# Performance work log

Hardware: AMD Instinct MI355X
Metric: run time of the kernel (lower is better)

The kernel has to match this reference:

```python
import jax, jax.numpy as jnp
import numpy as np

N = 20000      # nodes
E = 320000     # edges (avg degree 16)
S = 2          # extra feature axis (mean-pooled before fc)
IN = 128       # in_feats
H = 246        # n_hidden (must be 246 to match fc = Linear(246, 1))


def setup_inputs() -> dict:
    key = jax.random.key(0)
    ks = jax.random.split(key, 8)
    feat = jax.random.normal(ks[0], (N, S, IN), jnp.float32)
    src = jax.random.randint(ks[1], (E,), 0, N, jnp.int32)
    dst = jax.random.randint(ks[2], (E,), 0, N, jnp.int32)
    glorot = lambda k, shp, fan: jax.random.normal(k, shp, jnp.float32) / np.sqrt(fan).astype(np.float32)
    return {
        "features": feat,
        "src": src,
        "dst": dst,
        "W0": glorot(ks[3], (IN, H), IN), "b0": jnp.zeros((H,), jnp.float32),
        "W1": glorot(ks[4], (H, H), H),   "b1": jnp.zeros((H,), jnp.float32),
        "W2": glorot(ks[5], (H, H), H),   "b2": jnp.zeros((H,), jnp.float32),
        "fc_w": glorot(ks[6], (H, 1), H), "fc_b": jnp.zeros((1,), jnp.float32),
    }


def reference(features, src, dst, W0, b0, W1, b1, W2, b2, fc_w, fc_b):
    # DGL GraphConv, norm='both': h' = act( D_in^{-1/2} A D_out^{-1/2} h W + b )
    ones = jnp.ones((src.shape[0],), jnp.float32)
    out_deg = jax.ops.segment_sum(ones, src, num_segments=N)
    in_deg = jax.ops.segment_sum(ones, dst, num_segments=N)
    norm_out = jax.lax.rsqrt(jnp.maximum(out_deg, 1.0))[:, None, None]  # [N,1,1]
    norm_in = jax.lax.rsqrt(jnp.maximum(in_deg, 1.0))[:, None, None]

    def graph_conv(h, W, b):
        h = h * norm_out                                      # [N,S,F] scale by src-side norm
        agg = jax.ops.segment_sum(h[src], dst, num_segments=N)  # gather->scatter-add over edges
        agg = agg * norm_in
        return jax.nn.relu(agg @ W + b)

    h = graph_conv(features.astype(jnp.float32), W0, b0)
    # dropout between layers is identity in eval mode
    h = graph_conv(h, W1, b1)
    h = graph_conv(h, W2, b2)
    return h.mean(axis=1) @ fc_w + fc_b  # [N,1]
```

## Files before the change

kernel.cpp:

```cpp
#include <hip/hip_runtime.h>
#include <hip/hip_fp16.h>

#define NN 20000
#define NE 320000
#define SS 2
#define FIN 128
#define FH 246

typedef _Float16 f16x8 __attribute__((ext_vector_type(8)));
typedef float f32x4 __attribute__((ext_vector_type(4)));

__global__ void degree_kernel(const int* __restrict__ src, const int* __restrict__ dst,
                              int* __restrict__ deg_out, int* __restrict__ deg_in) {
    int e = blockIdx.x * blockDim.x + threadIdx.x;
    if (e < NE) {
        atomicAdd(&deg_out[src[e]], 1);
        atomicAdd(&deg_in[dst[e]], 1);
    }
}

__global__ void norm_kernel(const int* __restrict__ deg_out, const int* __restrict__ deg_in,
                            float* __restrict__ norm_out, float* __restrict__ norm_in) {
    int n = blockIdx.x * blockDim.x + threadIdx.x;
    if (n < NN) {
        norm_out[n] = rsqrtf(fmaxf((float)deg_out[n], 1.0f));
        norm_in[n]  = rsqrtf(fmaxf((float)deg_in[n], 1.0f));
    }
}

__global__ void alloc_kernel(const int* __restrict__ deg_in, int* __restrict__ row_start,
                             int* __restrict__ cursor, int* __restrict__ counter) {
    __shared__ int smem[256];
    __shared__ int base_s;
    int tid = threadIdx.x;
    int i = blockIdx.x * 256 + tid;
    int v = (i < NN) ? deg_in[i] : 0;
    smem[tid] = v;
    __syncthreads();
    for (int off = 1; off < 256; off <<= 1) {
        int t = (tid >= off) ? smem[tid - off] : 0;
        __syncthreads();
        smem[tid] += t;
        __syncthreads();
    }
    int incl = smem[tid];
    if (tid == 0) base_s = atomicAdd(counter, smem[255]);
    __syncthreads();
    if (i < NN) {
        int excl = base_s + incl - v;
        row_start[i] = excl;
        cursor[i]    = excl;
    }
}

__global__ void scatter_kernel(const int* __restrict__ src, const int* __restrict__ dst,
                               int* __restrict__ cursor, int* __restrict__ sorted_src) {
    int e = blockIdx.x * blockDim.x + threadIdx.x;
    if (e < NE) {
        int d = dst[e];
        int pos = atomicAdd(&cursor[d], 1);
        sorted_src[pos] = src[e];
    }
}

__global__ void convert_w_split(const float* __restrict__ W,
                                ushort* __restrict__ Wh, ushort* __restrict__ Wl, int K) {
    int n = blockIdx.x, k = threadIdx.x;
    float v = (k < K && n < 246) ? W[k * 246 + n] : 0.f;
    _Float16 h = (_Float16)v;
    _Float16 l = (_Float16)(v - (float)h);
    Wh[n * 256 + k] = *(ushort*)&h;
    Wl[n * 256 + k] = *(ushort*)&l;
}

__global__ void init_out(float* __restrict__ out, const float* __restrict__ fcb) {
    int i = blockIdx.x * 256 + threadIdx.x;
    if (i < NN) out[i] = fcb[0];
}

template<int F4ROW>
__global__ void aggregate2(const float* __restrict__ h,
                           const int* __restrict__ row_start,
                           const int* __restrict__ deg_in,
                           const int* __restrict__ sorted_src,
                           const float* __restrict__ norm_out,
                           const float* __restrict__ norm_in,
                           ushort* __restrict__ Ah, ushort* __restrict__ Al) {
    int g  = threadIdx.x >> 5;
    int l  = threadIdx.x & 31;
    int n  = blockIdx.x * 4 + g;
    if (n >= NN) return;
    int idx = blockIdx.y * 32 + l;
    const float4* hv = (const float4*)h;
    int beg = row_start[n];
    int end = beg + deg_in[n];
    float4 acc = {0.f, 0.f, 0.f, 0.f};
    int i = beg;
    for (; i + 4 <= end; i += 4) {
        int s0 = sorted_src[i + 0];
        int s1 = sorted_src[i + 1];
        int s2 = sorted_src[i + 2];
        int s3 = sorted_src[i + 3];
        float n0 = norm_out[s0], n1 = norm_out[s1];
        float n2 = norm_out[s2], n3 = norm_out[s3];
        float4 v0 = hv[(size_t)s0 * F4ROW + idx];
        float4 v1 = hv[(size_t)s1 * F4ROW + idx];
        float4 v2 = hv[(size_t)s2 * F4ROW + idx];
        float4 v3 = hv[(size_t)s3 * F4ROW + idx];
        acc.x += v0.x * n0 + v1.x * n1 + v2.x * n2 + v3.x * n3;
        acc.y += v0.y * n0 + v1.y * n1 + v2.y * n2 + v3.y * n3;
        acc.z += v0.z * n0 + v1.z * n1 + v2.z * n2 + v3.z * n3;
        acc.w += v0.w * n0 + v1.w * n1 + v2.w * n2 + v3.w * n3;
    }
    for (; i < end; ++i) {
        int s = sorted_src[i];
        float nr = norm_out[s];
        float4 v = hv[(size_t)s * F4ROW + idx];
        acc.x += v.x * nr;
        acc.y += v.y * nr;
        acc.z += v.z * nr;
        acc.w += v.w * nr;
    }
    float ni = norm_in[n];
    float v[4] = {acc.x * ni, acc.y * ni, acc.z * ni, acc.w * ni};
    ushort hp[4], lp[4];
#pragma unroll
    for (int j = 0; j < 4; ++j) {
        _Float16 hh = (_Float16)v[j];
        _Float16 ll = (_Float16)(v[j] - (float)hh);
        hp[j] = *(ushort*)&hh;
        lp[j] = *(ushort*)&ll;
    }
    ((uint2*)Ah)[(size_t)n * F4ROW + idx] = *(uint2*)hp;
    ((uint2*)Al)[(size_t)n * F4ROW + idx] = *(uint2*)lp;
}

template<int KP, bool FUSE>
__global__ __launch_bounds__(256) void gemm_split(const ushort* __restrict__ Ah,
                                                  const ushort* __restrict__ Al,
                                                  const ushort* __restrict__ Wh,
                                                  const ushort* __restrict__ Wl,
                                                  const float* __restrict__ b,
                                                  void* __restrict__ outv,
                                                  const float* __restrict__ fcw) {
    constexpr int NT = KP / 32;
    constexpr int AS = KP / 8;
    __shared__ __align__(16) _Float16 Ah_s[64][40];
    __shared__ __align__(16) _Float16 Al_s[64][40];
    __shared__ __align__(16) _Float16 Bh_s[128][40];
    __shared__ __align__(16) _Float16 Bl_s[128][40];

    int tid  = threadIdx.x;
    int m0   = blockIdx.x * 64;
    int n0   = blockIdx.y * 128;
    int wave = tid >> 6, lane = tid & 63;
    int wm = wave >> 1, wn = wave & 1;
    int lr = lane & 15, quad = lane >> 4;

    f32x4 acc[2][4];
#pragma unroll
    for (int mi = 0; mi < 2; ++mi)
#pragma unroll
        for (int ni = 0; ni < 4; ++ni) acc[mi][ni] = {0.f, 0.f, 0.f, 0.f};

    int ar = tid >> 2;
    int aq = tid & 3;
    const uint4* Ahv = (const uint4*)Ah;
    const uint4* Alv = (const uint4*)Al;
    const uint4* Whv = (const uint4*)Wh;
    const uint4* Wlv = (const uint4*)Wl;

    for (int t0 = 0; t0 < NT; ++t0) {
        size_t abase = (size_t)(m0 + ar) * AS + t0 * 4 + aq;
        *(uint4*)&Ah_s[ar][aq * 8] = Ahv[abase];
        *(uint4*)&Al_s[ar][aq * 8] = Alv[abase];
#pragma unroll
        for (int it = 0; it < 2; ++it) {
            int f = it * 256 + tid;
            int rn = f >> 2, q = f & 3;
            size_t base = (size_t)(n0 + rn) * 32 + t0 * 4 + q;
            *(uint4*)&Bh_s[rn][q * 8] = Whv[base];
            *(uint4*)&Bl_s[rn][q * 8] = Wlv[base];
        }
        __syncthreads();

        f16x8 ah[2], al[2], bh[4], bl[4];
#pragma unroll
        for (int mi = 0; mi < 2; ++mi) {
            ah[mi] = *(const f16x8*)&Ah_s[wm * 32 + mi * 16 + lr][quad * 8];
            al[mi] = *(const f16x8*)&Al_s[wm * 32 + mi * 16 + lr][quad * 8];
        }
#pragma unroll
        for (int ni = 0; ni < 4; ++ni) {
            bh[ni] = *(const f16x8*)&Bh_s[wn * 64 + ni * 16 + lr][quad * 8];
            bl[ni] = *(const f16x8*)&Bl_s[wn * 64 + ni * 16 + lr][quad * 8];
        }
#pragma unroll
        for (int mi = 0; mi < 2; ++mi)
#pragma unroll
            for (int ni = 0; ni < 4; ++ni) {
                acc[mi][ni] = __builtin_amdgcn_mfma_f32_16x16x32_f16(ah[mi], bh[ni], acc[mi][ni], 0, 0, 0);
                acc[mi][ni] = __builtin_amdgcn_mfma_f32_16x16x32_f16(al[mi], bh[ni], acc[mi][ni], 0, 0, 0);
                acc[mi][ni] = __builtin_amdgcn_mfma_f32_16x16x32_f16(ah[mi], bl[ni], acc[mi][ni], 0, 0, 0);
            }
        __syncthreads();
    }

    if (FUSE) {
        float* out = (float*)outv;
#pragma unroll
        for (int mi = 0; mi < 2; ++mi) {
#pragma unroll
            for (int i = 0; i < 4; ++i) {
                float p = 0.f;
#pragma unroll
                for (int ni = 0; ni < 4; ++ni) {
                    int c = n0 + wn * 64 + ni * 16 + lr;
                    if (c < 246)
                        p += fmaxf(acc[mi][ni][i] + b[c], 0.f) * fcw[c];
                }
#pragma unroll
                for (int off = 8; off > 0; off >>= 1)
                    p += __shfl_down(p, off, 16);
                if (lr == 0) {
                    int m = m0 + wm * 32 + mi * 16 + quad * 4 + i;
                    atomicAdd(&out[m >> 1], 0.5f * p);
                }
            }
        }
    } else {
        float* outF = (float*)outv;
#pragma unroll
        for (int ni = 0; ni < 4; ++ni) {
            int c = n0 + wn * 64 + ni * 16 + lr;
            float bj = (c < 246) ? b[c] : 0.f;
#pragma unroll
            for (int mi = 0; mi < 2; ++mi)
#pragma unroll
                for (int i = 0; i < 4; ++i) {
                    int m = m0 + wm * 32 + mi * 16 + quad * 4 + i;
                    outF[(size_t)m * 256 + c] = fmaxf(acc[mi][ni][i] + bj, 0.f);
                }
        }
    }
}

extern "C" void kernel_launch(void* const* d_in, const int* in_sizes, int n_in,
                              void* d_out, int out_size, void* d_ws, size_t ws_size,
                              hipStream_t stream) {
    const float* feat = (const float*)d_in[0];
    const int*   src  = (const int*)d_in[1];
    const int*   dst  = (const int*)d_in[2];
    const float* W0   = (const float*)d_in[3];
    const float* b0   = (const float*)d_in[4];
    const float* W1   = (const float*)d_in[5];
    const float* b1   = (const float*)d_in[6];
    const float* W2   = (const float*)d_in[7];
    const float* b2   = (const float*)d_in[8];
    const float* fcw  = (const float*)d_in[9];
    const float* fcb  = (const float*)d_in[10];
    float* out = (float*)d_out;

    char* ws = (char*)d_ws;
    size_t off = 0;
    auto alloc = [&](size_t bytes) {
        void* p = ws + off;
        off = (off + bytes + 255) & ~(size_t)255;
        return p;
    };
    int*    deg_out_i = (int*)alloc((2 * NN + 64) * sizeof(int));
    int*    deg_in_i  = deg_out_i + NN;
    int*    counter   = deg_out_i + 2 * NN;
    int*    row_start = (int*)alloc(NN * sizeof(int));
    int*    cursor    = (int*)alloc(NN * sizeof(int));
    int*    sorted    = (int*)alloc(NE * sizeof(int));
    float*  norm_out  = (float*)alloc(NN * sizeof(float));
    float*  norm_in   = (float*)alloc(NN * sizeof(float));
    ushort* Wh0 = (ushort*)alloc(256 * 256 * sizeof(ushort));
    ushort* Wl0 = (ushort*)alloc(256 * 256 * sizeof(ushort));
    ushort* Wh1 = (ushort*)alloc(256 * 256 * sizeof(ushort));
    ushort* Wl1 = (ushort*)alloc(256 * 256 * sizeof(ushort));
    ushort* Wh2 = (ushort*)alloc(256 * 256 * sizeof(ushort));
    ushort* Wl2 = (ushort*)alloc(256 * 256 * sizeof(ushort));
    ushort* Ahb = (ushort*)alloc((size_t)NN * SS * 256 * sizeof(ushort));
    ushort* Alb = (ushort*)alloc((size_t)NN * SS * 256 * sizeof(ushort));
    float*  bufH = (float*)alloc((size_t)NN * SS * 256 * sizeof(float));

    hipMemsetAsync(deg_out_i, 0, (2 * NN + 1) * sizeof(int), stream);

    degree_kernel<<<(NE + 255) / 256, 256, 0, stream>>>(src, dst, deg_out_i, deg_in_i);
    norm_kernel<<<(NN + 255) / 256, 256, 0, stream>>>(deg_out_i, deg_in_i, norm_out, norm_in);
    alloc_kernel<<<(NN + 255) / 256, 256, 0, stream>>>(deg_in_i, row_start, cursor, counter);
    scatter_kernel<<<(NE + 255) / 256, 256, 0, stream>>>(src, dst, cursor, sorted);

    convert_w_split<<<256, 256, 0, stream>>>(W0, Wh0, Wl0, FIN);
    convert_w_split<<<256, 256, 0, stream>>>(W1, Wh1, Wl1, FH);
    convert_w_split<<<256, 256, 0, stream>>>(W2, Wh2, Wl2, FH);
    init_out<<<(NN + 255) / 256, 256, 0, stream>>>(out, fcb);

    const int NB = (NN + 3) / 4;
    dim3 ggrid(NN * SS / 64, 2);

    aggregate2<64><<<dim3(NB, 2), 128, 0, stream>>>(feat, row_start, deg_in_i, sorted,
                                                    norm_out, norm_in, Ahb, Alb);
    gemm_split<FIN, false><<<ggrid, 256, 0, stream>>>(Ahb, Alb, Wh0, Wl0, b0, bufH, fcw);

    aggregate2<128><<<dim3(NB, 4), 128, 0, stream>>>(bufH, row_start, deg_in_i, sorted,
                                                     norm_out, norm_in, Ahb, Alb);
    gemm_split<256, false><<<ggrid, 256, 0, stream>>>(Ahb, Alb, Wh1, Wl1, b1, bufH, fcw);

    aggregate2<128><<<dim3(NB, 4), 128, 0, stream>>>(bufH, row_start, deg_in_i, sorted,
                                                     norm_out, norm_in, Ahb, Alb);
    gemm_split<256, true><<<ggrid, 256, 0, stream>>>(Ahb, Alb, Wh2, Wl2, b2, out, fcw);
}
```

Measured before the change: 411.5 us.

## Make GEMM persistent with weight slab resident in LDS, fuse small setup kernels

Replaces the tiled GEMM, which reloads A and B tiles into shared memory every K step, with a persistent kernel. Each 512-thread block loads its full 128-column weight slab (hi and lo halves) into LDS once. Each wave then streams 32-row A tiles straight from global memory into registers, prefetching the next K slice, with no per-step barriers. It also folds the norm computation into the prefix-sum kernel and merges the three weight conversions into one launch, cutting launch count. The trade-offs are large LDS use (about 135 KB at K=256), fixed grid sizing of 128x2 blocks, and uncoalesced direct global A loads.

After: 661.7 us. +60.8%, slower.

```diff
diff --git a/kernel.cpp b/kernel.cpp
--- a/kernel.cpp
+++ b/kernel.cpp
@@ -19,17 +19,10 @@
     }
 }
 
-__global__ void norm_kernel(const int* __restrict__ deg_out, const int* __restrict__ deg_in,
-                            float* __restrict__ norm_out, float* __restrict__ norm_in) {
-    int n = blockIdx.x * blockDim.x + threadIdx.x;
-    if (n < NN) {
-        norm_out[n] = rsqrtf(fmaxf((float)deg_out[n], 1.0f));
-        norm_in[n]  = rsqrtf(fmaxf((float)deg_in[n], 1.0f));
-    }
-}
-
-__global__ void alloc_kernel(const int* __restrict__ deg_in, int* __restrict__ row_start,
-                             int* __restrict__ cursor, int* __restrict__ counter) {
+__global__ void alloc_kernel(const int* __restrict__ deg_out, const int* __restrict__ deg_in,
+                             float* __restrict__ norm_out, float* __restrict__ norm_in,
+                             int* __restrict__ row_start, int* __restrict__ cursor,
+                             int* __restrict__ counter) {
     __shared__ int smem[256];
     __shared__ int base_s;
     int tid = threadIdx.x;
@@ -50,6 +43,8 @@
         int excl = base_s + incl - v;
         row_start[i] = excl;
         cursor[i]    = excl;
+        norm_out[i] = rsqrtf(fmaxf((float)deg_out[i], 1.0f));
+        norm_in[i]  = rsqrtf(fmaxf((float)v, 1.0f));
     }
 }
 
@@ -63,9 +58,16 @@
     }
 }
 
-__global__ void convert_w_split(const float* __restrict__ W,
-                                ushort* __restrict__ Wh, ushort* __restrict__ Wl, int K) {
+__global__ void convert_w_all(const float* __restrict__ W0, const float* __restrict__ W1,
+                              const float* __restrict__ W2,
+                              ushort* __restrict__ Wh0, ushort* __restrict__ Wl0,
+                              ushort* __restrict__ Wh1, ushort* __restrict__ Wl1,
+                              ushort* __restrict__ Wh2, ushort* __restrict__ Wl2) {
     int n = blockIdx.x, k = threadIdx.x;
+    const float* W; ushort* Wh; ushort* Wl; int K;
+    if (blockIdx.y == 0)      { W = W0; Wh = Wh0; Wl = Wl0; K = FIN; }
+    else if (blockIdx.y == 1) { W = W1; Wh = Wh1; Wl = Wl1; K = FH; }
+    else                      { W = W2; Wh = Wh2; Wl = Wl2; K = FH; }
     float v = (k < K && n < 246) ? W[k * 246 + n] : 0.f;
     _Float16 h = (_Float16)v;
     _Float16 l = (_Float16)(v - (float)h);
@@ -136,111 +138,124 @@
 }
 
 template<int KP, bool FUSE>
-__global__ __launch_bounds__(256) void gemm_split(const ushort* __restrict__ Ah,
-                                                  const ushort* __restrict__ Al,
-                                                  const ushort* __restrict__ Wh,
-                                                  const ushort* __restrict__ Wl,
-                                                  const float* __restrict__ b,
-                                                  void* __restrict__ outv,
-                                                  const float* __restrict__ fcw) {
+__global__ __launch_bounds__(512) void gemm_persist(const ushort* __restrict__ Ah,
+                                                    const ushort* __restrict__ Al,
+                                                    const ushort* __restrict__ Wh,
+                                                    const ushort* __restrict__ Wl,
+                                                    const float* __restrict__ b,
+                                                    void* __restrict__ outv,
+                                                    const float* __restrict__ fcw) {
     constexpr int NT = KP / 32;
-    constexpr int AS = KP / 8;
-    __shared__ __align__(16) _Float16 Ah_s[64][40];
-    __shared__ __align__(16) _Float16 Al_s[64][40];
-    __shared__ __align__(16) _Float16 Bh_s[128][40];
-    __shared__ __align__(16) _Float16 Bl_s[128][40];
+    constexpr int R4 = KP / 8;
+    __shared__ __align__(16) _Float16 Bh_s[128][KP + 8];
+    __shared__ __align__(16) _Float16 Bl_s[128][KP + 8];
 
     int tid  = threadIdx.x;
-    int m0   = blockIdx.x * 64;
     int n0   = blockIdx.y * 128;
     int wave = tid >> 6, lane = tid & 63;
-    int wm = wave >> 1, wn = wave & 1;
     int lr = lane & 15, quad = lane >> 4;
 
-    f32x4 acc[2][4];
-#pragma unroll
-    for (int mi = 0; mi < 2; ++mi)
-#pragma unroll
-        for (int ni = 0; ni < 4; ++ni) acc[mi][ni] = {0.f, 0.f, 0.f, 0.f};
-
-    int ar = tid >> 2;
-    int aq = tid & 3;
+    const uint4* Whv = (const uint4*)Wh;
+    const uint4* Wlv = (const uint4*)Wl;
+#pragma unroll
+    for (int it = 0; it < (128 * R4) / 512; ++it) {
+        int f  = it * 512 + tid;
+        int rn = f / R4, q = f % R4;
+        size_t base = (size_t)(n0 + rn) * 32 + q;
+        *(uint4*)&Bh_s[rn][q * 8] = Whv[base];
+        *(uint4*)&Bl_s[rn][q * 8] = Wlv[base];
+    }
+    __syncthreads();
+
     const uint4* Ahv = (const uint4*)Ah;
     const uint4* Alv = (const uint4*)Al;
-    const uint4* Whv = (const uint4*)Wh;
-    const uint4* Wlv = (const uint4*)Wl;
-
-    for (int t0 = 0; t0 < NT; ++t0) {
-        size_t abase = (size_t)(m0 + ar) * AS + t0 * 4 + aq;
-        *(uint4*)&Ah_s[ar][aq * 8] = Ahv[abase];
-        *(uint4*)&Al_s[ar][aq * 8] = Alv[abase];
-#pragma unroll
-        for (int it = 0; it < 2; ++it) {
-            int f = it * 256 + tid;
-            int rn = f >> 2, q = f & 3;
-            size_t base = (size_t)(n0 + rn) * 32 + t0 * 4 + q;
-            *(uint4*)&Bh_s[rn][q * 8] = Whv[base];
-            *(uint4*)&Bl_s[rn][q * 8] = Wlv[base];
+
+    for (int t = blockIdx.x * 8 + wave; t < (NN * SS) / 32; t += 128 * 8) {
+        int tb = t * 32;
+        f32x4 acc[2][8];
+#pragma unroll
+        for (int mi = 0; mi < 2; ++mi)
+#pragma unroll
+            for (int ni = 0; ni < 8; ++ni) acc[mi][ni] = {0.f, 0.f, 0.f, 0.f};
+
+        size_t arow[2];
+#pragma unroll
+        for (int mi = 0; mi < 2; ++mi)
+            arow[mi] = (size_t)(tb + mi * 16 + lr) * R4 + quad;
+
+        uint4 cah[2], cal[2];
+#pragma unroll
+        for (int mi = 0; mi < 2; ++mi) {
+            cah[mi] = Ahv[arow[mi]];
+            cal[mi] = Alv[arow[mi]];
         }
-        __syncthreads();
-
-        f16x8 ah[2], al[2], bh[4], bl[4];
-#pragma unroll
-        for (int mi = 0; mi < 2; ++mi) {
-            ah[mi] = *(const f16x8*)&Ah_s[wm * 32 + mi * 16 + lr][quad * 8];
-            al[mi] = *(const f16x8*)&Al_s[wm * 32 + mi * 16 + lr][quad * 8];
+        for (int t0 = 0; t0 < NT; ++t0) {
+            uint4 nah[2], nal[2];
+            if (t0 + 1 < NT) {
+#pragma unroll
+                for (int mi = 0; mi < 2; ++mi) {
+                    nah[mi] = Ahv[arow[mi] + (t0 + 1) * 4];
+                    nal[mi] = Alv[arow[mi] + (t0 + 1) * 4];
+                }
+            }
+            f16x8 ahf[2], alf[2];
+#pragma unroll
+            for (int mi = 0; mi < 2; ++mi) {
+                ahf[mi] = *(f16x8*)&cah[mi];
+                alf[mi] = *(f16x8*)&cal[mi];
+            }
+            int ko = t0 * 32 + quad * 8;
+#pragma unroll
+            for (int ni = 0; ni < 8; ++ni) {
+                f16x8 bh = *(const f16x8*)&Bh_s[ni * 16 + lr][ko];
+                f16x8 bl = *(const f16x8*)&Bl_s[ni * 16 + lr][ko];
+                acc[0][ni] = __builtin_amdgcn_mfma_f32_16x16x32_f16(ahf[0], bh, acc[0][ni], 0, 0, 0);
+                acc[1][ni] = __builtin_amdgcn_mfma_f32_16x16x32_f16(ahf[1], bh, acc[1][ni], 0, 0, 0);
+                acc[0][ni] = __builtin_amdgcn_mfma_f32_16x16x32_f16(alf[0], bh, acc[0][ni], 0, 0, 0);
+                acc[1][ni] = __builtin_amdgcn_mfma_f32_16x16x32_f16(alf[1], bh, acc[1][ni], 0, 0, 0);
+                acc[0][ni] = __builtin_amdgcn_mfma_f32_16x16x32_f16(ahf[0], bl, acc[0][ni], 0, 0, 0);
+                acc[1][ni] = __builtin_amdgcn_mfma_f32_16x16x32_f16(ahf[1], bl, acc[1][ni], 0, 0, 0);
+            }
+#pragma unroll
+            for (int mi = 0; mi < 2; ++mi) { cah[mi] = nah[mi]; cal[mi] = nal[mi]; }
         }
-#pragma unroll
-        for (int ni = 0; ni < 4; ++ni) {
-            bh[ni] = *(const f16x8*)&Bh_s[wn * 64 + ni * 16 + lr][quad * 8];
-            bl[ni] = *(const f16x8*)&Bl_s[wn * 64 + ni * 16 + lr][quad * 8];
-        }
-#pragma unroll
-        for (int mi = 0; mi < 2; ++mi)
-#pragma unroll
-            for (int ni = 0; ni < 4; ++ni) {
-                acc[mi][ni] = __builtin_amdgcn_mfma_f32_16x16x32_f16(ah[mi], bh[ni], acc[mi][ni], 0, 0, 0);
-                acc[mi][ni] = __builtin_amdgcn_mfma_f32_16x16x32_f16(al[mi], bh[ni], acc[mi][ni], 0, 0, 0);
-                acc[mi][ni] = __builtin_amdgcn_mfma_f32_16x16x32_f16(ah[mi], bl[ni], acc[mi][ni], 0, 0, 0);
-            }
-        __syncthreads();
-    }
-
-    if (FUSE) {
-        float* out = (float*)outv;
-#pragma unroll
-        for (int mi = 0; mi < 2; ++mi) {
-#pragma unroll
-            for (int i = 0; i < 4; ++i) {
-                float p = 0.f;
-#pragma unroll
-                for (int ni = 0; ni < 4; ++ni) {
-                    int c = n0 + wn * 64 + ni * 16 + lr;
-                    if (c < 246)
-                        p += fmaxf(acc[mi][ni][i] + b[c], 0.f) * fcw[c];
+
+        if (FUSE) {
+            float* out = (float*)outv;
+#pragma unroll
+            for (int mi = 0; mi < 2; ++mi) {
+#pragma unroll
+                for (int i = 0; i < 4; ++i) {
+                    float p = 0.f;
+#pragma unroll
+                    for (int ni = 0; ni < 8; ++ni) {
+                        int c = n0 + ni * 16 + lr;
+                        if (c < 246)
+                            p += fmaxf(acc[mi][ni][i] + b[c], 0.f) * fcw[c];
+                    }
+#pragma unroll
+                    for (int off = 8; off > 0; off >>= 1)
+                        p += __shfl_down(p, off, 16);
+                    if (lr == 0) {
+                        int m = tb + mi * 16 + quad * 4 + i;
+                        atomicAdd(&out[m >> 1], 0.5f * p);
+                    }
                 }
-#pragma unroll
-                for (int off = 8; off > 0; off >>= 1)
-                    p += __shfl_down(p, off, 16);
-                if (lr == 0) {
-                    int m = m0 + wm * 32 + mi * 16 + quad * 4 + i;
-                    atomicAdd(&out[m >> 1], 0.5f * p);
-                }
-            }
-        }
-    } else {
-        float* outF = (float*)outv;
-#pragma unroll
-        for (int ni = 0; ni < 4; ++ni) {
-            int c = n0 + wn * 64 + ni * 16 + lr;
-            float bj = (c < 246) ? b[c] : 0.f;
-#pragma unroll
-            for (int mi = 0; mi < 2; ++mi)
-#pragma unroll
-                for (int i = 0; i < 4; ++i) {
-                    int m = m0 + wm * 32 + mi * 16 + quad * 4 + i;
-                    outF[(size_t)m * 256 + c] = fmaxf(acc[mi][ni][i] + bj, 0.f);
-                }
+            }
+        } else {
+            float* outF = (float*)outv;
+#pragma unroll
+            for (int ni = 0; ni < 8; ++ni) {
+                int c = n0 + ni * 16 + lr;
+                float bj = (c < 246) ? b[c] : 0.f;
+#pragma unroll
+                for (int mi = 0; mi < 2; ++mi)
+#pragma unroll
+                    for (int i = 0; i < 4; ++i) {
+                        int m = tb + mi * 16 + quad * 4 + i;
+                        outF[(size_t)m * 256 + c] = fmaxf(acc[mi][ni][i] + bj, 0.f);
+                    }
+            }
         }
     }
 }
@@ -289,27 +304,25 @@
     hipMemsetAsync(deg_out_i, 0, (2 * NN + 1) * sizeof(int), stream);
 
     degree_kernel<<<(NE + 255) / 256, 256, 0, stream>>>(src, dst, deg_out_i, deg_in_i);
-    norm_kernel<<<(NN + 255) / 256, 256, 0, stream>>>(deg_out_i, deg_in_i, norm_out, norm_in);
-    alloc_kernel<<<(NN + 255) / 256, 256, 0, stream>>>(deg_in_i, row_start, cursor, counter);
+    alloc_kernel<<<(NN + 255) / 256, 256, 0, stream>>>(deg_out_i, deg_in_i, norm_out, norm_in,
+                                                       row_start, cursor, counter);
     scatter_kernel<<<(NE + 255) / 256, 256, 0, stream>>>(src, dst, cursor, sorted);
 
-    convert_w_split<<<256, 256, 0, stream>>>(W0, Wh0, Wl0, FIN);
-    convert_w_split<<<256, 256, 0, stream>>>(W1, Wh1, Wl1, FH);
-    convert_w_split<<<256, 256, 0, stream>>>(W2, Wh2, Wl2, FH);
+    convert_w_all<<<dim3(256, 3), 256, 0, stream>>>(W0, W1, W2, Wh0, Wl0, Wh1, Wl1, Wh2, Wl2);
     init_out<<<(NN + 255) / 256, 256, 0, stream>>>(out, fcb);
 
     const int NB = (NN + 3) / 4;
-    dim3 ggrid(NN * SS / 64, 2);
+    dim3 pgrid(128, 2);
 
     aggregate2<64><<<dim3(NB, 2), 128, 0, stream>>>(feat, row_start, deg_in_i, sorted,
                                                     norm_out, norm_in, Ahb, Alb);
-    gemm_split<FIN, false><<<ggrid, 256, 0, stream>>>(Ahb, Alb, Wh0, Wl0, b0, bufH, fcw);
+    gemm_persist<FIN, false><<<pgrid, 512, 0, stream>>>(Ahb, Alb, Wh0, Wl0, b0, bufH, fcw);
 
     aggregate2<128><<<dim3(NB, 4), 128, 0, stream>>>(bufH, row_start, deg_in_i, sorted,
                                                      norm_out, norm_in, Ahb, Alb);
-    gemm_split<256, false><<<ggrid, 256, 0, stream>>>(Ahb, Alb, Wh1, Wl1, b1, bufH, fcw);
+    gemm_persist<256, false><<<pgrid, 512, 0, stream>>>(Ahb, Alb, Wh1, Wl1, b1, bufH, fcw);
 
     aggregate2<128><<<dim3(NB, 4), 128, 0, stream>>>(bufH, row_start, deg_in_i, sorted,
                                                      norm_out, norm_in, Ahb, Alb);
-    gemm_split<256, true><<<ggrid, 256, 0, stream>>>(Ahb, Alb, Wh2, Wl2, b2, out, fcw);
-}
+    gemm_persist<256, true><<<pgrid, 512, 0, stream>>>(Ahb, Alb, Wh2, Wl2, b2, out, fcw);
+}
```

## Fuse setup kernels and remap aggregation to 16-lane node groups

Applied to the files above, without the earlier changes.

The norm computation is folded into the prefix-sum allocation kernel, and the three weight-split conversions are merged into one launch over a 3-deep grid, cutting launch count. The aggregation kernel now gives each node a 16-lane group covering 8 nodes per block, with the feature chunk encoded in a flattened 1D block index so the chunks of one node set sit next to each other. This is meant to improve locality of the gathered source rows and index reads across neighbouring blocks. In exchange, each thread has fewer independent lanes per node and the grid becomes larger.

Measured after the change: 369.3 us, median of 2. -10.2%, faster.

```diff
diff --git a/kernel.cpp b/kernel.cpp
--- a/kernel.cpp
+++ b/kernel.cpp
@@ -19,17 +19,10 @@
     }
 }
 
-__global__ void norm_kernel(const int* __restrict__ deg_out, const int* __restrict__ deg_in,
-                            float* __restrict__ norm_out, float* __restrict__ norm_in) {
-    int n = blockIdx.x * blockDim.x + threadIdx.x;
-    if (n < NN) {
-        norm_out[n] = rsqrtf(fmaxf((float)deg_out[n], 1.0f));
-        norm_in[n]  = rsqrtf(fmaxf((float)deg_in[n], 1.0f));
-    }
-}
-
-__global__ void alloc_kernel(const int* __restrict__ deg_in, int* __restrict__ row_start,
-                             int* __restrict__ cursor, int* __restrict__ counter) {
+__global__ void alloc_kernel(const int* __restrict__ deg_out, const int* __restrict__ deg_in,
+                             float* __restrict__ norm_out, float* __restrict__ norm_in,
+                             int* __restrict__ row_start, int* __restrict__ cursor,
+                             int* __restrict__ counter) {
     __shared__ int smem[256];
     __shared__ int base_s;
     int tid = threadIdx.x;
@@ -50,6 +43,8 @@
         int excl = base_s + incl - v;
         row_start[i] = excl;
         cursor[i]    = excl;
+        norm_out[i] = rsqrtf(fmaxf((float)deg_out[i], 1.0f));
+        norm_in[i]  = rsqrtf(fmaxf((float)v, 1.0f));
     }
 }
 
@@ -63,9 +58,16 @@
     }
 }
 
-__global__ void convert_w_split(const float* __restrict__ W,
-                                ushort* __restrict__ Wh, ushort* __restrict__ Wl, int K) {
+__global__ void convert_w_all(const float* __restrict__ W0, const float* __restrict__ W1,
+                              const float* __restrict__ W2,
+                              ushort* __restrict__ Wh0, ushort* __restrict__ Wl0,
+                              ushort* __restrict__ Wh1, ushort* __restrict__ Wl1,
+                              ushort* __restrict__ Wh2, ushort* __restrict__ Wl2) {
     int n = blockIdx.x, k = threadIdx.x;
+    const float* W; ushort* Wh; ushort* Wl; int K;
+    if (blockIdx.y == 0)      { W = W0; Wh = Wh0; Wl = Wl0; K = FIN; }
+    else if (blockIdx.y == 1) { W = W1; Wh = Wh1; Wl = Wl1; K = FH; }
+    else                      { W = W2; Wh = Wh2; Wl = Wl2; K = FH; }
     float v = (k < K && n < 246) ? W[k * 246 + n] : 0.f;
     _Float16 h = (_Float16)v;
     _Float16 l = (_Float16)(v - (float)h);
@@ -78,7 +80,7 @@
     if (i < NN) out[i] = fcb[0];
 }
 
-template<int F4ROW>
+template<int F4ROW, int NCH>
 __global__ void aggregate2(const float* __restrict__ h,
                            const int* __restrict__ row_start,
                            const int* __restrict__ deg_in,
@@ -86,11 +88,13 @@
                            const float* __restrict__ norm_out,
                            const float* __restrict__ norm_in,
                            ushort* __restrict__ Ah, ushort* __restrict__ Al) {
-    int g  = threadIdx.x >> 5;
-    int l  = threadIdx.x & 31;
-    int n  = blockIdx.x * 4 + g;
+    int g  = threadIdx.x >> 4;
+    int l  = threadIdx.x & 15;
+    int cb = blockIdx.x & (NCH - 1);
+    int nb = blockIdx.x / NCH;
+    int n  = nb * 8 + g;
     if (n >= NN) return;
-    int idx = blockIdx.y * 32 + l;
+    int idx = cb * 16 + l;
     const float4* hv = (const float4*)h;
     int beg = row_start[n];
     int end = beg + deg_in[n];
@@ -289,27 +293,25 @@
     hipMemsetAsync(deg_out_i, 0, (2 * NN + 1) * sizeof(int), stream);
 
     degree_kernel<<<(NE + 255) / 256, 256, 0, stream>>>(src, dst, deg_out_i, deg_in_i);
-    norm_kernel<<<(NN + 255) / 256, 256, 0, stream>>>(deg_out_i, deg_in_i, norm_out, norm_in);
-    alloc_kernel<<<(NN + 255) / 256, 256, 0, stream>>>(deg_in_i, row_start, cursor, counter);
+    alloc_kernel<<<(NN + 255) / 256, 256, 0, stream>>>(deg_out_i, deg_in_i, norm_out, norm_in,
+                                                       row_start, cursor, counter);
     scatter_kernel<<<(NE + 255) / 256, 256, 0, stream>>>(src, dst, cursor, sorted);
 
-    convert_w_split<<<256, 256, 0, stream>>>(W0, Wh0, Wl0, FIN);
-    convert_w_split<<<256, 256, 0, stream>>>(W1, Wh1, Wl1, FH);
-    convert_w_split<<<256, 256, 0, stream>>>(W2, Wh2, Wl2, FH);
+    convert_w_all<<<dim3(256, 3), 256, 0, stream>>>(W0, W1, W2, Wh0, Wl0, Wh1, Wl1, Wh2, Wl2);
     init_out<<<(NN + 255) / 256, 256, 0, stream>>>(out, fcb);
 
-    const int NB = (NN + 3) / 4;
+    const int NB8 = (NN + 7) / 8;
     dim3 ggrid(NN * SS / 64, 2);
 
-    aggregate2<64><<<dim3(NB, 2), 128, 0, stream>>>(feat, row_start, deg_in_i, sorted,
+    aggregate2<64, 4><<<NB8 * 4, 128, 0, stream>>>(feat, row_start, deg_in_i, sorted,
+                                                   norm_out, norm_in, Ahb, Alb);
+    gemm_split<FIN, false><<<ggrid, 256, 0, stream>>>(Ahb, Alb, Wh0, Wl0, b0, bufH, fcw);
+
+    aggregate2<128, 8><<<NB8 * 8, 128, 0, stream>>>(bufH, row_start, deg_in_i, sorted,
                                                     norm_out, norm_in, Ahb, Alb);
-    gemm_split<FIN, false><<<ggrid, 256, 0, stream>>>(Ahb, Alb, Wh0, Wl0, b0, bufH, fcw);
-
-    aggregate2<128><<<dim3(NB, 4), 128, 0, stream>>>(bufH, row_start, deg_in_i, sorted,
-                                                     norm_out, norm_in, Ahb, Alb);
     gemm_split<256, false><<<ggrid, 256, 0, stream>>>(Ahb, Alb, Wh1, Wl1, b1, bufH, fcw);
 
-    aggregate2<128><<<dim3(NB, 4), 128, 0, stream>>>(bufH, row_start, deg_in_i, sorted,
-                                                     norm_out, norm_in, Ahb, Alb);
+    aggregate2<128, 8><<<NB8 * 8, 128, 0, stream>>>(bufH, row_start, deg_in_i, sorted,
+                                                    norm_out, norm_in, Ahb, Alb);
     gemm_split<256, true><<<ggrid, 256, 0, stream>>>(Ahb, Alb, Wh2, Wl2, b2, out, fcw);
 }
```
